# Kernel tuning notes

Measured on AMD Instinct MI355X. Metric: run time of the kernel, lower is better.

The kernel has to match this reference:

```python
import jax, jax.numpy as jnp
import numpy as np

C_IN = 34   # C*V = 2*17 channels after reshape
C_MID = 16
C_OUT = 3
N_LAYERS = 3
BN_EPS = 1e-5
NEG_SLOPE = 0.01


def setup_inputs() -> dict:
    key = jax.random.key(0)
    ks = jax.random.split(key, 16)
    B, C, T, V = 512, 2, 2048, 17
    s = 1.0 / np.sqrt(C_IN)
    inp = {
        "x": jax.random.normal(ks[0], (B, C, T, V), dtype=jnp.float32),
        # stacked per-layer 1x1-conv (linear) weights for Q/K/V of 3 attention layers
        "wq": jax.random.normal(ks[1], (N_LAYERS, C_IN, C_IN), dtype=jnp.float32) * s,
        "bq": jax.random.normal(ks[2], (N_LAYERS, C_IN), dtype=jnp.float32) * 0.02,
        "wk": jax.random.normal(ks[3], (N_LAYERS, C_IN, C_IN), dtype=jnp.float32) * s,
        "bk": jax.random.normal(ks[4], (N_LAYERS, C_IN), dtype=jnp.float32) * 0.02,
        "wv": jax.random.normal(ks[5], (N_LAYERS, C_IN, C_IN), dtype=jnp.float32) * s,
        "bv": jax.random.normal(ks[6], (N_LAYERS, C_IN), dtype=jnp.float32) * 0.02,
        # head: conv1 -> BN -> LeakyReLU -> conv2
        "w1": jax.random.normal(ks[7], (C_MID, C_IN), dtype=jnp.float32) * s,
        "b1": jax.random.normal(ks[8], (C_MID,), dtype=jnp.float32) * 0.02,
        "gamma": jnp.ones((C_MID,), dtype=jnp.float32),
        "beta": jnp.zeros((C_MID,), dtype=jnp.float32),
        "mean": jax.random.normal(ks[9], (C_MID,), dtype=jnp.float32) * 0.1,
        "var": jax.random.uniform(ks[10], (C_MID,), dtype=jnp.float32, minval=0.5, maxval=1.5),
        "w2": jax.random.normal(ks[11], (C_OUT, C_MID), dtype=jnp.float32) * (1.0 / np.sqrt(C_MID)),
        "b2": jax.random.normal(ks[12], (C_OUT,), dtype=jnp.float32) * 0.02,
    }
    return inp


def _conv1x1(w, b, h):
    # 1x1 Conv1d == linear over channel dim: (O,C) x (B,C,T) -> (B,O,T)
    return jnp.einsum('oc,bct->bot', w, h) + b[:, None]


def reference(x, wq, bq, wk, bk, wv, bv, w1, b1, gamma, beta, mean, var, w2, b2):
    B, C, T, V = x.shape
    h = x.transpose(0, 1, 3, 2).reshape(B, C * V, T)  # (B, 34, T)
    scale = 1.0 / (T ** 0.5)  # K.size(-1) ** 0.5 in the original
    for i in range(N_LAYERS):
        Q = _conv1x1(wq[i], bq[i], h)
        K = _conv1x1(wk[i], bk[i], h)
        Vv = _conv1x1(wv[i], bv[i], h)
        scores = jnp.einsum('bct,bdt->bcd', Q, K) * scale  # (B, 34, 34) channel attention
        attn = jax.nn.softmax(scores, axis=-1)
        h = jnp.einsum('bcd,bdt->bct', attn, Vv)
    y = _conv1x1(w1, b1, h)                               # (B, 16, T)
    inv = gamma / jnp.sqrt(var + BN_EPS)                  # inference-mode BatchNorm1d
    y = (y - mean[:, None]) * inv[:, None] + beta[:, None]
    y = jnp.where(y > 0, y, NEG_SLOPE * y)                # LeakyReLU
    return _conv1x1(w2, b2, y)                            # (B, 3, T)
```

## Files before the change

### kernel.cpp

```cpp
#include <hip/hip_runtime.h>

#define CV   34
#define TTOT 2048
#define NB   512
#define XB   69632
#define XC   34816

#define GS_STRIDE 1192
#define RB_OFF    (512 * 1192)
#define RB_STRIDE 576

typedef __attribute__((ext_vector_type(8))) short v8s;
typedef __attribute__((ext_vector_type(4))) float v4f;

__device__ __forceinline__ unsigned short f2bf(float f) {
    unsigned int u = __float_as_uint(f);
    u = u + 0x7FFFu + ((u >> 16) & 1u);
    return (unsigned short)(u >> 16);
}
__device__ __forceinline__ float bf2f(unsigned short s) {
    return __uint_as_float(((unsigned int)s) << 16);
}

__device__ __forceinline__ unsigned int cvtpk_bf16(float a, float b) {
    unsigned int r;
    asm("v_cvt_pk_bf16_f32 %0, %1, %2" : "=v"(r) : "v"(a), "v"(b));
    return r;
}

__device__ __forceinline__ void split8(const float (&f)[8], v8s* hi, v8s* lo) {
    union { unsigned int u[4]; v8s s; } H, L;
#pragma unroll
    for (int p = 0; p < 4; ++p) {
        float a = f[2 * p], b = f[2 * p + 1];
        unsigned int h = cvtpk_bf16(a, b);
        float ra = a - __uint_as_float(h << 16);
        float rb = b - __uint_as_float(h & 0xFFFF0000u);
        L.u[p] = cvtpk_bf16(ra, rb);
        H.u[p] = h;
    }
    *hi = H.s;
    *lo = L.s;
}

__device__ __forceinline__ void stage_chunk(const float* __restrict__ xb, int t0,
                                            float* rawbuf, int w, int lane) {
#pragma unroll
    for (int i = 0; i < 5; ++i) {
        int idx = i * 4 + w;
        if (idx < 17) {
            int fl = idx * 256 + lane * 4;
            int co = (fl >= 2176) ? 1 : 0;
            const float* g = xb + t0 * 17 + fl + co * 32640;
            __builtin_amdgcn_global_load_lds(
                (const __attribute__((address_space(1))) void*)g,
                (__attribute__((address_space(3))) void*)(rawbuf + idx * 256),
                16, 0, 0);
        }
    }
}

struct SmemGramB {
    float Gpart[4][34][36];
    float spart[4][36];
};

__global__ __launch_bounds__(256, 4) void k_gram(const float* __restrict__ x,
                                                 float* __restrict__ ws) {
    __shared__ __align__(16) union {
        float raw[2][4352];
        SmemGramB b;
    } sm;

    const int b    = blockIdx.x >> 2;
    const int seg  = blockIdx.x & 3;
    const int tid  = threadIdx.x;
    const int l    = tid & 63;
    const int w    = tid >> 6;
    const int row16 = l & 15;
    const int quad  = l >> 4;
    const float* xb = x + (size_t)b * XB;
    const int t0 = seg * 512;

    int offc[3];
#pragma unroll
    for (int r = 0; r < 3; ++r) {
        int c = r * 16 + row16;
        if (c > 33) c = 33;
        offc[r] = (c >= 17) ? (2159 + c) : c;
    }
    const int koff = w * 32 + quad * 8;

    v4f accG[3][3];
    v4f accS[3];
    v4f vz = {0.f, 0.f, 0.f, 0.f};
#pragma unroll
    for (int r = 0; r < 3; ++r) {
        accS[r] = vz;
#pragma unroll
        for (int c = 0; c < 3; ++c) accG[r][c] = vz;
    }
    v8s ones;
#pragma unroll
    for (int i = 0; i < 8; ++i) ones[i] = (short)0x3F80;

    stage_chunk(xb, t0, sm.raw[0], w, l);
    __syncthreads();

    for (int ch = 0; ch < 4; ++ch) {
        const int cur = ch & 1;
        if (ch < 3) stage_chunk(xb, t0 + (ch + 1) * 128, sm.raw[cur ^ 1], w, l);

        const float* rb = sm.raw[cur] + koff * 17;
        v8s fh[3], fl4[3];
#pragma unroll
        for (int r = 0; r < 3; ++r) {
            const float* p = rb + offc[r];
            float f[8];
#pragma unroll
            for (int e = 0; e < 8; ++e) f[e] = p[e * 17];
            split8(f, &fh[r], &fl4[r]);
        }
#pragma unroll
        for (int r = 0; r < 3; ++r) {
#pragma unroll
            for (int c = 0; c < 3; ++c) {
                accG[r][c] = __builtin_amdgcn_mfma_f32_16x16x32_bf16(fh[r],  fh[c],  accG[r][c], 0, 0, 0);
                accG[r][c] = __builtin_amdgcn_mfma_f32_16x16x32_bf16(fh[r],  fl4[c], accG[r][c], 0, 0, 0);
                accG[r][c] = __builtin_amdgcn_mfma_f32_16x16x32_bf16(fl4[r], fh[c],  accG[r][c], 0, 0, 0);
            }
            accS[r] = __builtin_amdgcn_mfma_f32_16x16x32_bf16(fh[r],  ones, accS[r], 0, 0, 0);
            accS[r] = __builtin_amdgcn_mfma_f32_16x16x32_bf16(fl4[r], ones, accS[r], 0, 0, 0);
        }
        __syncthreads();
    }

#pragma unroll
    for (int r = 0; r < 3; ++r) {
#pragma unroll
        for (int c = 0; c < 3; ++c) {
#pragma unroll
            for (int i = 0; i < 4; ++i) {
                int m = r * 16 + quad * 4 + i;
                int n = c * 16 + row16;
                if (m < 34 && n < 34) sm.b.Gpart[w][m][n] = accG[r][c][i];
            }
        }
        if (row16 == 0) {
#pragma unroll
            for (int i = 0; i < 4; ++i) {
                int m = r * 16 + quad * 4 + i;
                if (m < 34) sm.b.spart[w][m] = accS[r][i];
            }
        }
    }
    __syncthreads();
    float* gout = ws + (size_t)b * GS_STRIDE;
    for (int idx = tid; idx < 1156; idx += 256) {
        int m = idx / 34, n = idx - m * 34;
        atomicAdd(&gout[idx], sm.b.Gpart[0][m][n] + sm.b.Gpart[1][m][n] +
                              sm.b.Gpart[2][m][n] + sm.b.Gpart[3][m][n]);
    }
    if (tid < 34)
        atomicAdd(&gout[1156 + tid], sm.b.spart[0][tid] + sm.b.spart[1][tid] +
                                     sm.b.spart[2][tid] + sm.b.spart[3][tid]);
}


__device__ __forceinline__ void mm24(const float L[][36], const float R[][36],
                                     float D[][36], int u) {
    int ti = u / 9, tj = u - ti * 9;
    int i0 = ti * 2, j0 = tj * 4;
    float acc[2][4] = {};
    for (int e0 = 0; e0 < 36; e0 += 4) {
        float4 lv[2], rv[4];
        lv[0] = *(const float4*)&L[i0][e0];
        lv[1] = *(const float4*)&L[i0 + 1][e0];
#pragma unroll
        for (int c = 0; c < 4; ++c) rv[c] = *(const float4*)&R[j0 + c][e0];
#pragma unroll
        for (int a = 0; a < 2; ++a)
#pragma unroll
            for (int c = 0; c < 4; ++c)
                acc[a][c] += lv[a].x * rv[c].x + lv[a].y * rv[c].y +
                             lv[a].z * rv[c].z + lv[a].w * rv[c].w;
    }
#pragma unroll
    for (int a = 0; a < 2; ++a)
#pragma unroll
        for (int c = 0; c < 4; ++c) D[i0 + a][j0 + c] = acc[a][c];
}

__device__ __forceinline__ void mmG4(const float* __restrict__ Lg,
                                     const float R[][36], float D[][36],
                                     int transpose, int u) {
    int ti = u / 9, tj = u - ti * 9;
    int i0 = ti * 4, j0 = tj * 4;
    float acc[4][4] = {};
    for (int e0 = 0; e0 < 32; e0 += 4) {
        float2 la[4], lb[4];
        float4 rv[4];
#pragma unroll
        for (int a = 0; a < 4; ++a) {
            int ri = i0 + a; ri = ri < 34 ? ri : 33;
            la[a] = *(const float2*)(Lg + ri * 34 + e0);
            lb[a] = *(const float2*)(Lg + ri * 34 + e0 + 2);
        }
#pragma unroll
        for (int c = 0; c < 4; ++c) rv[c] = *(const float4*)&R[j0 + c][e0];
#pragma unroll
        for (int a = 0; a < 4; ++a)
#pragma unroll
            for (int c = 0; c < 4; ++c)
                acc[a][c] += la[a].x * rv[c].x + la[a].y * rv[c].y +
                             lb[a].x * rv[c].z + lb[a].y * rv[c].w;
    }
    {
        float2 la[4];
#pragma unroll
        for (int a = 0; a < 4; ++a) {
            int ri = i0 + a; ri = ri < 34 ? ri : 33;
            la[a] = *(const float2*)(Lg + ri * 34 + 32);
        }
#pragma unroll
        for (int c = 0; c < 4; ++c) {
            float r0 = R[j0 + c][32], r1 = R[j0 + c][33];
#pragma unroll
            for (int a = 0; a < 4; ++a) acc[a][c] += la[a].x * r0 + la[a].y * r1;
        }
    }
#pragma unroll
    for (int a = 0; a < 4; ++a) {
        if (i0 + a < 34) {
#pragma unroll
            for (int c = 0; c < 4; ++c) {
                if (transpose) D[j0 + c][i0 + a] = acc[a][c];
                else           D[i0 + a][j0 + c] = acc[a][c];
            }
        }
    }
}

__global__ __launch_bounds__(256) void k_chain(
    const float* __restrict__ wq, const float* __restrict__ bq,
    const float* __restrict__ wk, const float* __restrict__ bk,
    const float* __restrict__ wv, const float* __restrict__ bv,
    const float* __restrict__ w1, const float* __restrict__ b1,
    const float* __restrict__ gamma, const float* __restrict__ beta,
    const float* __restrict__ mean, const float* __restrict__ var,
    float* __restrict__ ws) {
    __shared__ float G0b[36][36], At[36][36], Aq[36][36], Ak[36][36],
        AvT[36][36], S1[36][36], Sc[36][36];
    __shared__ float s0v[36], a_[36], aq_[36], ak_[36], avv_[36],
        qs_[36], ks_[36], invv[16];

    const int tid = threadIdx.x;
    const int b   = blockIdx.x;
    const float* gsb = ws + (size_t)b * GS_STRIDE;

    for (int i = tid; i < 1296; i += 256) {
        int m = i / 36, n = i - m * 36;
        G0b[m][n] = 0; At[m][n] = 0; Aq[m][n] = 0; Ak[m][n] = 0;
        AvT[m][n] = 0; S1[m][n] = 0; Sc[m][n] = 0;
    }
    if (tid < 36) {
        s0v[tid] = 0; a_[tid] = 0; aq_[tid] = 0; ak_[tid] = 0; avv_[tid] = 0;
        qs_[tid] = 0; ks_[tid] = 0;
    }
    __syncthreads();
    for (int i = tid; i < 1156; i += 256) {
        int m = i / 34, n = i - m * 34;
        G0b[m][n] = gsb[i];
        Aq[m][n] = wq[i]; Ak[m][n] = wk[i]; AvT[n][m] = wv[i];
    }
    if (tid < 34) {
        s0v[tid] = gsb[1156 + tid];
        aq_[tid] = bq[tid]; ak_[tid] = bk[tid]; avv_[tid] = bv[tid];
    }
    __syncthreads();

    for (int lyr = 0; lyr < 3; ++lyr) {
        const float* wql = wq + lyr * 1156;
        const float* wkl = wk + lyr * 1156;
        const float* wvl = wv + lyr * 1156;
        if (lyr > 0) {
            if (tid < 243) {
                int g = tid / 81, u = tid - g * 81;
                const float* Lg = (g == 0) ? wql : (g == 1) ? wkl : wvl;
                float (*D)[36] = (g == 0) ? Aq : (g == 1) ? Ak : AvT;
                mmG4(Lg, At, D, g == 2, u);
            }
            __syncthreads();
        }
        if (tid < 153) {
            mm24(Aq, G0b, S1, tid);
        } else if (lyr > 0 && tid < 255) {
            int u = tid - 153, r = u / 34, c = u - r * 34;
            const float* wrow = ((r == 0) ? wql : (r == 1) ? wkl : wvl) + c * 34;
            float s = 0;
            for (int e = 0; e < 34; ++e) s += wrow[e] * a_[e];
            float bb = (r == 0) ? bq[lyr * 34 + c]
                     : (r == 1) ? bk[lyr * 34 + c] : bv[lyr * 34 + c];
            if (r == 0) aq_[c] = s + bb;
            else if (r == 1) ak_[c] = s + bb;
            else avv_[c] = s + bb;
        }
        __syncthreads();
        if (tid < 153) {
            mm24(S1, Ak, Sc, tid);
        } else if (tid >= 160 && tid < 228) {
            int u = tid - 160, r = u / 34, c = u - r * 34;
            const float (*M)[36] = r ? Ak : Aq;
            float s = 0;
            for (int e = 0; e < 34; ++e) s += M[c][e] * s0v[e];
            if (r == 0) qs_[c] = s; else ks_[c] = s;
        }
        __syncthreads();
        if (tid < 34) {
            const int c = tid;
            const float scale = 0.022097086912079608f;
            float mx = -1e30f;
            for (int d = 0; d < 34; ++d) {
                float v = (Sc[c][d] + qs_[c] * ak_[d] + aq_[c] * ks_[d] +
                           2048.0f * aq_[c] * ak_[d]) * scale;
                Sc[c][d] = v;
                mx = fmaxf(mx, v);
            }
            float sum = 0;
            for (int d = 0; d < 34; ++d) {
                float e = __expf(Sc[c][d] - mx);
                Sc[c][d] = e;
                sum += e;
            }
            float rs = 1.0f / sum;
            for (int d = 0; d < 34; ++d) Sc[c][d] *= rs;
        }
        __syncthreads();
        if (tid < 153) {
            mm24(AvT, Sc, At, tid);
        } else if (tid >= 160 && tid < 194) {
            int c = tid - 160;
            float s = 0;
            for (int d = 0; d < 34; ++d) s += Sc[c][d] * avv_[d];
            a_[c] = s;
        }
        __syncthreads();
    }

    if (tid < 72) {
        int ti = tid / 9, tj = tid - ti * 9;
        int i0 = ti * 2, j0 = tj * 4;
        float acc[2][4] = {};
        for (int e0 = 0; e0 < 32; e0 += 4) {
            float2 la[2], lb[2];
            float4 rv[4];
#pragma unroll
            for (int a = 0; a < 2; ++a) {
                la[a] = *(const float2*)(w1 + (i0 + a) * 34 + e0);
                lb[a] = *(const float2*)(w1 + (i0 + a) * 34 + e0 + 2);
            }
#pragma unroll
            for (int c = 0; c < 4; ++c) rv[c] = *(const float4*)&At[j0 + c][e0];
#pragma unroll
            for (int a = 0; a < 2; ++a)
#pragma unroll
                for (int c = 0; c < 4; ++c)
                    acc[a][c] += la[a].x * rv[c].x + la[a].y * rv[c].y +
                                 lb[a].x * rv[c].z + lb[a].y * rv[c].w;
        }
        {
            float2 la[2];
#pragma unroll
            for (int a = 0; a < 2; ++a)
                la[a] = *(const float2*)(w1 + (i0 + a) * 34 + 32);
#pragma unroll
            for (int c = 0; c < 4; ++c) {
                float r0 = At[j0 + c][32], r1 = At[j0 + c][33];
#pragma unroll
                for (int a = 0; a < 2; ++a) acc[a][c] += la[a].x * r0 + la[a].y * r1;
            }
        }
#pragma unroll
        for (int a = 0; a < 2; ++a)
#pragma unroll
            for (int c = 0; c < 4; ++c) S1[i0 + a][j0 + c] = acc[a][c];
    } else if (tid < 88) {
        int o = tid - 72;
        invv[o] = gamma[o] * rsqrtf(var[o] + 1e-5f);
    } else if (tid < 104) {
        int o = tid - 88;
        float s = 0;
        for (int e = 0; e < 34; ++e) s += w1[o * 34 + e] * a_[e];
        ks_[o] = s + b1[o];
    }
    __syncthreads();
    float* wb = ws + RB_OFF + (size_t)b * RB_STRIDE;
    if (tid < 16) {
        wb[512 + tid] = (ks_[tid] - mean[tid]) * invv[tid] + beta[tid];
    } else if (tid < 48) {
        int u = tid - 16, o = u & 15, cc = u >> 4;
        wb[528 + cc * 16 + o] = S1[o][32 + cc] * invv[o];
    }
    unsigned short* wp = (unsigned short*)wb;
    for (int i = tid; i < 512; i += 256) {
        int o = i >> 5, c = i & 31;
        float vv = S1[o][c] * invv[o];
        unsigned short hb = f2bf(vv);
        wp[i] = hb;
        wp[512 + i] = f2bf(vv - bf2f(hb));
    }
}

__global__ __launch_bounds__(256, 4) void k_out(const float* __restrict__ x,
                                                const float* __restrict__ w2,
                                                const float* __restrict__ b2,
                                                const float* __restrict__ ws,
                                                float* __restrict__ out) {
    __shared__ __align__(16) float raw[2][4352];

    const int tid  = threadIdx.x;
    const int b    = blockIdx.x >> 3;
    const int seg  = (blockIdx.x & 7) * 256;
    const int l    = tid & 63;
    const int w    = tid >> 6;
    const int quad = l >> 4;
    const int col  = l & 15;

    const float* wb = ws + RB_OFF + (size_t)b * RB_STRIDE;
    const unsigned short* wp = (const unsigned short*)wb;
    v8s aH = *(const v8s*)&wp[col * 32 + quad * 8];
    v8s aL = *(const v8s*)&wp[512 + col * 32 + quad * 8];
    float cyr[4], w2r[3][4], wy32r[4], wy33r[4];
#pragma unroll
    for (int i = 0; i < 4; ++i) {
        int o = quad * 4 + i;
        cyr[i]   = wb[512 + o];
        wy32r[i] = wb[528 + o];
        wy33r[i] = wb[544 + o];
#pragma unroll
        for (int p = 0; p < 3; ++p) w2r[p][i] = w2[p * 16 + o];
    }
    float b2r[3] = {b2[0], b2[1], b2[2]};
    const float* xb = x + (size_t)b * XB;

    int offq[8];
#pragma unroll
    for (int e = 0; e < 8; ++e) {
        int c = quad * 8 + e;
        offq[e] = (c >= 17) ? (2159 + c) : c;
    }

    stage_chunk(xb, seg, raw[0], w, l);
    __syncthreads();

    for (int ch = 0; ch < 2; ++ch) {
        if (ch == 0) stage_chunk(xb, seg + 128, raw[1], w, l);
        for (int tt = w; tt < 8; tt += 4) {
            const int tl = tt * 16 + col;
            const float* rbt = raw[ch] + tl * 17;
            float f[8];
#pragma unroll
            for (int e = 0; e < 8; ++e) f[e] = rbt[offq[e]];
            v8s bH, bL;
            split8(f, &bH, &bL);
            v4f acc = {0.f, 0.f, 0.f, 0.f};
            acc = __builtin_amdgcn_mfma_f32_16x16x32_bf16(aH, bH, acc, 0, 0, 0);
            acc = __builtin_amdgcn_mfma_f32_16x16x32_bf16(aH, bL, acc, 0, 0, 0);
            acc = __builtin_amdgcn_mfma_f32_16x16x32_bf16(aL, bH, acc, 0, 0, 0);
            float h32 = rbt[2191];
            float h33 = rbt[2192];
            float op[3] = {0, 0, 0};
#pragma unroll
            for (int i = 0; i < 4; ++i) {
                float y = acc[i] + cyr[i] + wy32r[i] * h32 + wy33r[i] * h33;
                float z = (y > 0.f) ? y : 0.01f * y;
#pragma unroll
                for (int p = 0; p < 3; ++p) op[p] += w2r[p][i] * z;
            }
#pragma unroll
            for (int p = 0; p < 3; ++p) {
                op[p] += __shfl_xor(op[p], 16);
                op[p] += __shfl_xor(op[p], 32);
            }
            if (l < 16) {
                int tg = seg + ch * 128 + tt * 16 + l;
#pragma unroll
                for (int p = 0; p < 3; ++p)
                    out[((size_t)b * 3 + p) * 2048 + tg] = op[p] + b2r[p];
            }
        }
        __syncthreads();
    }
}

extern "C" void kernel_launch(void* const* d_in, const int* in_sizes, int n_in,
                              void* d_out, int out_size, void* d_ws, size_t ws_size,
                              hipStream_t stream) {
    const float* x     = (const float*)d_in[0];
    const float* wq    = (const float*)d_in[1];
    const float* bq    = (const float*)d_in[2];
    const float* wk    = (const float*)d_in[3];
    const float* bk    = (const float*)d_in[4];
    const float* wv    = (const float*)d_in[5];
    const float* bv    = (const float*)d_in[6];
    const float* w1    = (const float*)d_in[7];
    const float* b1    = (const float*)d_in[8];
    const float* gamma = (const float*)d_in[9];
    const float* beta  = (const float*)d_in[10];
    const float* mean  = (const float*)d_in[11];
    const float* var   = (const float*)d_in[12];
    const float* w2    = (const float*)d_in[13];
    const float* b2    = (const float*)d_in[14];
    float* ws  = (float*)d_ws;
    float* out = (float*)d_out;

    hipMemsetAsync(d_ws, 0, (size_t)NB * GS_STRIDE * sizeof(float), stream);
    k_gram<<<dim3(2048), dim3(256), 0, stream>>>(x, ws);
    k_chain<<<dim3(512), dim3(256), 0, stream>>>(wq, bq, wk, bk, wv, bv,
                                                 w1, b1, gamma, beta, mean, var, ws);
    k_out<<<dim3(4096), dim3(256), 0, stream>>>(x, w2, b2, ws, out);
}
```

Baseline: 312.2 us.

## Fold biases into augmented 35x35 matrices and run k_chain as one wave

Rewrites the per-batch small-matrix chain kernel to use a single 64-thread wave. Each lane computes a 9x3 tile of the 36x36 products. The bias vectors and the Gram row-sum are folded into an extra 35th row and column, so the separate vector side computations for qs, ks, aq, ak, avv and the head bias disappear. The goal is less synchronization and thread idling in a latency-bound tiny kernel, at the cost of fewer threads per block and more serial work per lane.

```diff
diff --git a/kernel.cpp b/kernel.cpp
--- a/kernel.cpp
+++ b/kernel.cpp
@@ -167,81 +167,96 @@
 }
 
 
-__device__ __forceinline__ void mm24(const float L[][36], const float R[][36],
-                                     float D[][36], int u) {
-    int ti = u / 9, tj = u - ti * 9;
-    int i0 = ti * 2, j0 = tj * 4;
-    float acc[2][4] = {};
+__device__ __forceinline__ void wave_mm(const float (*__restrict__ L)[36],
+                                        const float (*__restrict__ R)[36],
+                                        float (*__restrict__ D)[36], int l) {
+    const int lr = l >> 4, lc = l & 15;
+    const int i0 = lr * 9;
+    const bool has3 = (lc < 3);
+    const int j3 = has3 ? (lc + 32) : 0;
+    float a0[9], a1[9], a2[9];
+#pragma unroll
+    for (int a = 0; a < 9; ++a) { a0[a] = 0.f; a1[a] = 0.f; a2[a] = 0.f; }
+#pragma unroll
     for (int e0 = 0; e0 < 36; e0 += 4) {
-        float4 lv[2], rv[4];
-        lv[0] = *(const float4*)&L[i0][e0];
-        lv[1] = *(const float4*)&L[i0 + 1][e0];
-#pragma unroll
-        for (int c = 0; c < 4; ++c) rv[c] = *(const float4*)&R[j0 + c][e0];
-#pragma unroll
-        for (int a = 0; a < 2; ++a)
-#pragma unroll
-            for (int c = 0; c < 4; ++c)
-                acc[a][c] += lv[a].x * rv[c].x + lv[a].y * rv[c].y +
-                             lv[a].z * rv[c].z + lv[a].w * rv[c].w;
-    }
-#pragma unroll
-    for (int a = 0; a < 2; ++a)
-#pragma unroll
-        for (int c = 0; c < 4; ++c) D[i0 + a][j0 + c] = acc[a][c];
-}
-
-__device__ __forceinline__ void mmG4(const float* __restrict__ Lg,
-                                     const float R[][36], float D[][36],
-                                     int transpose, int u) {
-    int ti = u / 9, tj = u - ti * 9;
-    int i0 = ti * 4, j0 = tj * 4;
-    float acc[4][4] = {};
+        const float4 r0 = *(const float4*)&R[lc][e0];
+        const float4 r1 = *(const float4*)&R[lc + 16][e0];
+        const float4 r2 = *(const float4*)&R[j3][e0];
+#pragma unroll
+        for (int a = 0; a < 9; ++a) {
+            const float4 lv = *(const float4*)&L[i0 + a][e0];
+            a0[a] += lv.x * r0.x + lv.y * r0.y + lv.z * r0.z + lv.w * r0.w;
+            a1[a] += lv.x * r1.x + lv.y * r1.y + lv.z * r1.z + lv.w * r1.w;
+            a2[a] += lv.x * r2.x + lv.y * r2.y + lv.z * r2.z + lv.w * r2.w;
+        }
+    }
+#pragma unroll
+    for (int a = 0; a < 9; ++a) {
+        D[i0 + a][lc]      = a0[a];
+        D[i0 + a][lc + 16] = a1[a];
+        if (has3) D[i0 + a][lc + 32] = a2[a];
+    }
+}
+
+__device__ __forceinline__ void wave_mmG(const float* __restrict__ Wg, int nrows,
+                                         const float (*__restrict__ R)[36],
+                                         float (*__restrict__ D)[36],
+                                         int transpose, int l) {
+    const int lr = l >> 4, lc = l & 15;
+    const int i0 = lr * 9;
+    const bool has3 = (lc < 3);
+    const int j3 = has3 ? (lc + 32) : 0;
+    float a0[9], a1[9], a2[9];
+#pragma unroll
+    for (int a = 0; a < 9; ++a) { a0[a] = 0.f; a1[a] = 0.f; a2[a] = 0.f; }
+#pragma unroll
     for (int e0 = 0; e0 < 32; e0 += 4) {
-        float2 la[4], lb[4];
-        float4 rv[4];
-#pragma unroll
-        for (int a = 0; a < 4; ++a) {
-            int ri = i0 + a; ri = ri < 34 ? ri : 33;
-            la[a] = *(const float2*)(Lg + ri * 34 + e0);
-            lb[a] = *(const float2*)(Lg + ri * 34 + e0 + 2);
-        }
-#pragma unroll
-        for (int c = 0; c < 4; ++c) rv[c] = *(const float4*)&R[j0 + c][e0];
-#pragma unroll
-        for (int a = 0; a < 4; ++a)
-#pragma unroll
-            for (int c = 0; c < 4; ++c)
-                acc[a][c] += la[a].x * rv[c].x + la[a].y * rv[c].y +
-                             lb[a].x * rv[c].z + lb[a].y * rv[c].w;
+        const float4 r0 = *(const float4*)&R[lc][e0];
+        const float4 r1 = *(const float4*)&R[lc + 16][e0];
+        const float4 r2 = *(const float4*)&R[j3][e0];
+#pragma unroll
+        for (int a = 0; a < 9; ++a) {
+            const int i = i0 + a;
+            float2 la = make_float2(0.f, 0.f), lb = make_float2(0.f, 0.f);
+            if (i < nrows) {
+                la = *(const float2*)(Wg + i * 34 + e0);
+                lb = *(const float2*)(Wg + i * 34 + e0 + 2);
+            }
+            a0[a] += la.x * r0.x + la.y * r0.y + lb.x * r0.z + lb.y * r0.w;
+            a1[a] += la.x * r1.x + la.y * r1.y + lb.x * r1.z + lb.y * r1.w;
+            a2[a] += la.x * r2.x + la.y * r2.y + lb.x * r2.z + lb.y * r2.w;
+        }
     }
     {
-        float2 la[4];
-#pragma unroll
-        for (int a = 0; a < 4; ++a) {
-            int ri = i0 + a; ri = ri < 34 ? ri : 33;
-            la[a] = *(const float2*)(Lg + ri * 34 + 32);
-        }
-#pragma unroll
-        for (int c = 0; c < 4; ++c) {
-            float r0 = R[j0 + c][32], r1 = R[j0 + c][33];
-#pragma unroll
-            for (int a = 0; a < 4; ++a) acc[a][c] += la[a].x * r0 + la[a].y * r1;
-        }
-    }
-#pragma unroll
-    for (int a = 0; a < 4; ++a) {
-        if (i0 + a < 34) {
-#pragma unroll
-            for (int c = 0; c < 4; ++c) {
-                if (transpose) D[j0 + c][i0 + a] = acc[a][c];
-                else           D[i0 + a][j0 + c] = acc[a][c];
-            }
-        }
-    }
-}
-
-__global__ __launch_bounds__(256) void k_chain(
+        const float r00 = R[lc][32],      r01 = R[lc][33];
+        const float r10 = R[lc + 16][32], r11 = R[lc + 16][33];
+        const float r20 = R[j3][32],      r21 = R[j3][33];
+#pragma unroll
+        for (int a = 0; a < 9; ++a) {
+            const int i = i0 + a;
+            float2 la = make_float2(0.f, 0.f);
+            if (i < nrows) la = *(const float2*)(Wg + i * 34 + 32);
+            a0[a] += la.x * r00 + la.y * r01;
+            a1[a] += la.x * r10 + la.y * r11;
+            a2[a] += la.x * r20 + la.y * r21;
+        }
+    }
+#pragma unroll
+    for (int a = 0; a < 9; ++a) {
+        const int i = i0 + a;
+        if (transpose) {
+            D[lc][i]      = a0[a];
+            D[lc + 16][i] = a1[a];
+            if (has3) D[lc + 32][i] = a2[a];
+        } else {
+            D[i][lc]      = a0[a];
+            D[i][lc + 16] = a1[a];
+            if (has3) D[i][lc + 32] = a2[a];
+        }
+    }
+}
+
+__global__ __launch_bounds__(64) void k_chain(
     const float* __restrict__ wq, const float* __restrict__ bq,
     const float* __restrict__ wk, const float* __restrict__ bk,
     const float* __restrict__ wv, const float* __restrict__ bv,
@@ -249,162 +264,103 @@
     const float* __restrict__ gamma, const float* __restrict__ beta,
     const float* __restrict__ mean, const float* __restrict__ var,
     float* __restrict__ ws) {
-    __shared__ float G0b[36][36], At[36][36], Aq[36][36], Ak[36][36],
-        AvT[36][36], S1[36][36], Sc[36][36];
-    __shared__ float s0v[36], a_[36], aq_[36], ak_[36], avv_[36],
-        qs_[36], ks_[36], invv[16];
-
-    const int tid = threadIdx.x;
-    const int b   = blockIdx.x;
+    __shared__ float SM[7][36][36];
+    float (*G0b)[36] = SM[0];
+    float (*At )[36] = SM[1];
+    float (*Aq )[36] = SM[2];
+    float (*Ak )[36] = SM[3];
+    float (*AvT)[36] = SM[4];
+    float (*S1 )[36] = SM[5];
+    float (*Sc )[36] = SM[6];
+
+    const int l = threadIdx.x;
+    const int b = blockIdx.x;
     const float* gsb = ws + (size_t)b * GS_STRIDE;
 
-    for (int i = tid; i < 1296; i += 256) {
-        int m = i / 36, n = i - m * 36;
-        G0b[m][n] = 0; At[m][n] = 0; Aq[m][n] = 0; Ak[m][n] = 0;
-        AvT[m][n] = 0; S1[m][n] = 0; Sc[m][n] = 0;
-    }
-    if (tid < 36) {
-        s0v[tid] = 0; a_[tid] = 0; aq_[tid] = 0; ak_[tid] = 0; avv_[tid] = 0;
-        qs_[tid] = 0; ks_[tid] = 0;
-    }
-    __syncthreads();
-    for (int i = tid; i < 1156; i += 256) {
-        int m = i / 34, n = i - m * 34;
-        G0b[m][n] = gsb[i];
-        Aq[m][n] = wq[i]; Ak[m][n] = wk[i]; AvT[n][m] = wv[i];
-    }
-    if (tid < 34) {
-        s0v[tid] = gsb[1156 + tid];
-        aq_[tid] = bq[tid]; ak_[tid] = bk[tid]; avv_[tid] = bv[tid];
-    }
+    {
+        const float4 z = make_float4(0.f, 0.f, 0.f, 0.f);
+        float* base = &SM[0][0][0];
+        for (int i = l * 4; i < 9072; i += 256) *(float4*)(base + i) = z;
+    }
+    __syncthreads();
+    for (int idx = l; idx < 1156; idx += 64) {
+        int m = idx / 34, n = idx - m * 34;
+        G0b[m][n] = gsb[idx];
+        Aq[m][n] = wq[idx];
+        Ak[m][n] = wk[idx];
+        AvT[n][m] = wv[idx];
+    }
+    if (l < 34) {
+        float s = gsb[1156 + l];
+        G0b[34][l] = s;
+        G0b[l][34] = s;
+        Aq[l][34]  = bq[l];
+        Ak[l][34]  = bk[l];
+        AvT[34][l] = bv[l];
+    }
+    if (l == 0) G0b[34][34] = 2048.0f;
     __syncthreads();
 
     for (int lyr = 0; lyr < 3; ++lyr) {
-        const float* wql = wq + lyr * 1156;
-        const float* wkl = wk + lyr * 1156;
-        const float* wvl = wv + lyr * 1156;
         if (lyr > 0) {
-            if (tid < 243) {
-                int g = tid / 81, u = tid - g * 81;
-                const float* Lg = (g == 0) ? wql : (g == 1) ? wkl : wvl;
-                float (*D)[36] = (g == 0) ? Aq : (g == 1) ? Ak : AvT;
-                mmG4(Lg, At, D, g == 2, u);
-            }
+            const float* wql = wq + lyr * 1156;
+            const float* wkl = wk + lyr * 1156;
+            const float* wvl = wv + lyr * 1156;
+            wave_mmG(wql, 34, At, Aq, 0, l);
+            wave_mmG(wkl, 34, At, Ak, 0, l);
+            wave_mmG(wvl, 34, At, AvT, 1, l);
             __syncthreads();
-        }
-        if (tid < 153) {
-            mm24(Aq, G0b, S1, tid);
-        } else if (lyr > 0 && tid < 255) {
-            int u = tid - 153, r = u / 34, c = u - r * 34;
-            const float* wrow = ((r == 0) ? wql : (r == 1) ? wkl : wvl) + c * 34;
-            float s = 0;
-            for (int e = 0; e < 34; ++e) s += wrow[e] * a_[e];
-            float bb = (r == 0) ? bq[lyr * 34 + c]
-                     : (r == 1) ? bk[lyr * 34 + c] : bv[lyr * 34 + c];
-            if (r == 0) aq_[c] = s + bb;
-            else if (r == 1) ak_[c] = s + bb;
-            else avv_[c] = s + bb;
-        }
-        __syncthreads();
-        if (tid < 153) {
-            mm24(S1, Ak, Sc, tid);
-        } else if (tid >= 160 && tid < 228) {
-            int u = tid - 160, r = u / 34, c = u - r * 34;
-            const float (*M)[36] = r ? Ak : Aq;
-            float s = 0;
-            for (int e = 0; e < 34; ++e) s += M[c][e] * s0v[e];
-            if (r == 0) qs_[c] = s; else ks_[c] = s;
-        }
-        __syncthreads();
-        if (tid < 34) {
-            const int c = tid;
+            if (l < 34) {
+                Aq[l][34]  += bq[lyr * 34 + l];
+                Ak[l][34]  += bk[lyr * 34 + l];
+                AvT[34][l] += bv[lyr * 34 + l];
+            }
+            __syncthreads();
+        }
+        wave_mm(Aq, G0b, S1, l);
+        __syncthreads();
+        wave_mm(S1, Ak, Sc, l);
+        __syncthreads();
+        if (l < 34) {
+            float f[36];
+#pragma unroll
+            for (int e0 = 0; e0 < 36; e0 += 4)
+                *(float4*)&f[e0] = *(const float4*)&Sc[l][e0];
             const float scale = 0.022097086912079608f;
             float mx = -1e30f;
-            for (int d = 0; d < 34; ++d) {
-                float v = (Sc[c][d] + qs_[c] * ak_[d] + aq_[c] * ks_[d] +
-                           2048.0f * aq_[c] * ak_[d]) * scale;
-                Sc[c][d] = v;
-                mx = fmaxf(mx, v);
-            }
-            float sum = 0;
-            for (int d = 0; d < 34; ++d) {
-                float e = __expf(Sc[c][d] - mx);
-                Sc[c][d] = e;
-                sum += e;
-            }
+#pragma unroll
+            for (int d = 0; d < 34; ++d) { f[d] *= scale; mx = fmaxf(mx, f[d]); }
+            float sum = 0.f;
+#pragma unroll
+            for (int d = 0; d < 34; ++d) { float e = __expf(f[d] - mx); f[d] = e; sum += e; }
             float rs = 1.0f / sum;
-            for (int d = 0; d < 34; ++d) Sc[c][d] *= rs;
-        }
-        __syncthreads();
-        if (tid < 153) {
-            mm24(AvT, Sc, At, tid);
-        } else if (tid >= 160 && tid < 194) {
-            int c = tid - 160;
-            float s = 0;
-            for (int d = 0; d < 34; ++d) s += Sc[c][d] * avv_[d];
-            a_[c] = s;
-        }
-        __syncthreads();
-    }
-
-    if (tid < 72) {
-        int ti = tid / 9, tj = tid - ti * 9;
-        int i0 = ti * 2, j0 = tj * 4;
-        float acc[2][4] = {};
-        for (int e0 = 0; e0 < 32; e0 += 4) {
-            float2 la[2], lb[2];
-            float4 rv[4];
-#pragma unroll
-            for (int a = 0; a < 2; ++a) {
-                la[a] = *(const float2*)(w1 + (i0 + a) * 34 + e0);
-                lb[a] = *(const float2*)(w1 + (i0 + a) * 34 + e0 + 2);
-            }
-#pragma unroll
-            for (int c = 0; c < 4; ++c) rv[c] = *(const float4*)&At[j0 + c][e0];
-#pragma unroll
-            for (int a = 0; a < 2; ++a)
-#pragma unroll
-                for (int c = 0; c < 4; ++c)
-                    acc[a][c] += la[a].x * rv[c].x + la[a].y * rv[c].y +
-                                 lb[a].x * rv[c].z + lb[a].y * rv[c].w;
-        }
-        {
-            float2 la[2];
-#pragma unroll
-            for (int a = 0; a < 2; ++a)
-                la[a] = *(const float2*)(w1 + (i0 + a) * 34 + 32);
-#pragma unroll
-            for (int c = 0; c < 4; ++c) {
-                float r0 = At[j0 + c][32], r1 = At[j0 + c][33];
-#pragma unroll
-                for (int a = 0; a < 2; ++a) acc[a][c] += la[a].x * r0 + la[a].y * r1;
-            }
-        }
-#pragma unroll
-        for (int a = 0; a < 2; ++a)
-#pragma unroll
-            for (int c = 0; c < 4; ++c) S1[i0 + a][j0 + c] = acc[a][c];
-    } else if (tid < 88) {
-        int o = tid - 72;
-        invv[o] = gamma[o] * rsqrtf(var[o] + 1e-5f);
-    } else if (tid < 104) {
-        int o = tid - 88;
-        float s = 0;
-        for (int e = 0; e < 34; ++e) s += w1[o * 34 + e] * a_[e];
-        ks_[o] = s + b1[o];
-    }
+#pragma unroll
+            for (int d = 0; d < 34; ++d) f[d] *= rs;
+            f[34] = 0.f; f[35] = 0.f;
+#pragma unroll
+            for (int e0 = 0; e0 < 36; e0 += 4)
+                *(float4*)&Sc[l][e0] = *(const float4*)&f[e0];
+        }
+        __syncthreads();
+        wave_mm(AvT, Sc, At, l);
+        __syncthreads();
+    }
+
+    wave_mmG(w1, 16, At, S1, 0, l);
     __syncthreads();
     float* wb = ws + RB_OFF + (size_t)b * RB_STRIDE;
-    if (tid < 16) {
-        wb[512 + tid] = (ks_[tid] - mean[tid]) * invv[tid] + beta[tid];
-    } else if (tid < 48) {
-        int u = tid - 16, o = u & 15, cc = u >> 4;
-        wb[528 + cc * 16 + o] = S1[o][32 + cc] * invv[o];
+    if (l < 16) {
+        float iv = gamma[l] * rsqrtf(var[l] + 1e-5f);
+        float cyraw = S1[l][34] + b1[l];
+        wb[512 + l] = (cyraw - mean[l]) * iv + beta[l];
+        wb[528 + l] = S1[l][32] * iv;
+        wb[544 + l] = S1[l][33] * iv;
     }
     unsigned short* wp = (unsigned short*)wb;
-    for (int i = tid; i < 512; i += 256) {
+    for (int i = l; i < 512; i += 64) {
         int o = i >> 5, c = i & 31;
-        float vv = S1[o][c] * invv[o];
+        float iv = gamma[o] * rsqrtf(var[o] + 1e-5f);
+        float vv = S1[o][c] * iv;
         unsigned short hb = f2bf(vv);
         wp[i] = hb;
         wp[512 + i] = f2bf(vv - bf2f(hb));
@@ -516,7 +472,7 @@
 
     hipMemsetAsync(d_ws, 0, (size_t)NB * GS_STRIDE * sizeof(float), stream);
     k_gram<<<dim3(2048), dim3(256), 0, stream>>>(x, ws);
-    k_chain<<<dim3(512), dim3(256), 0, stream>>>(wq, bq, wk, bk, wv, bv,
-                                                 w1, b1, gamma, beta, mean, var, ws);
+    k_chain<<<dim3(512), dim3(64), 0, stream>>>(wq, bq, wk, bk, wv, bv,
+                                                w1, b1, gamma, beta, mean, var, ws);
     k_out<<<dim3(4096), dim3(256), 0, stream>>>(x, w2, b2, ws, out);
 }
```

New measurement: 345.0 us. +10.5%, slower.
